# Kernel optimization log

Measured on AMD Instinct MI355X. Metric: run time of the kernel, lower is better.

## Reference

```python
import jax, jax.numpy as jnp
import numpy as np

B, S, D = 1, 2048, 1024
F = 1408            # expert intermediate dim
E = 16              # num experts
K = 2               # top_k
CAP_FACTOR = 1.25


def _mlp(h, wg, wu, wd):
    # DeepSeek-style gated MLP (SwiGLU, no bias)
    return (jax.nn.silu(h @ wg) * (h @ wu)) @ wd


def setup_inputs() -> dict:
    key = jax.random.key(0)
    ks = jax.random.split(key, 10)
    sd = 0.02
    return {
        "x": jax.random.normal(ks[0], (B, S, D), jnp.float32),
        "router_w": jax.random.normal(ks[1], (D, E), jnp.float32) * sd,
        "router_b": jnp.zeros((E,), jnp.float32),
        "w_gate": jax.random.normal(ks[2], (E, D, F), jnp.float32) * sd,
        "w_up": jax.random.normal(ks[3], (E, D, F), jnp.float32) * sd,
        "w_down": jax.random.normal(ks[4], (E, F, D), jnp.float32) * sd,
        "sw_gate": jax.random.normal(ks[5], (D, F), jnp.float32) * sd,
        "sw_up": jax.random.normal(ks[6], (D, F), jnp.float32) * sd,
        "sw_down": jax.random.normal(ks[7], (F, D), jnp.float32) * sd,
    }


def reference(x, router_w, router_b, w_gate, w_up, w_down, sw_gate, sw_up, sw_down):
    b, s, d = x.shape
    N = b * s
    NK = N * K
    C = int(np.ceil(CAP_FACTOR * NK / E))  # per-expert capacity

    x_tokens = x.reshape(N, d)

    # Router: softmax -> top-k -> renormalize
    logits = x_tokens @ router_w + router_b           # [N, E]
    probs = jax.nn.softmax(logits, axis=-1)
    vals, idx = jax.lax.top_k(probs, K)               # [N, K]
    vals = vals / (jnp.sum(vals, axis=-1, keepdims=True) + 1e-9)
    idx_flat = idx.reshape(NK)                        # int expert ids
    vals_flat = vals.reshape(NK)

    # Position within each expert's buffer = rank in flattened (token, k) order.
    # Same math as (cumsum(one_hot)*one_hot).sum(-1)-1 in the original.
    oh_e = jax.nn.one_hot(idx_flat, E, dtype=x.dtype)             # [NK, E] (small)
    pos = (jnp.cumsum(oh_e, axis=0) * oh_e).sum(axis=1) - 1       # [NK]
    within = (pos < C).astype(x.dtype)                            # capacity mask
    pos_c = jnp.clip(pos, 0, C - 1).astype(jnp.int32)

    # Dispatch: scatter tokens into per-expert buffers. Positions are unique
    # per expert, so scatter-add equals the dense one-hot einsum exactly.
    token_ids = jnp.arange(NK) // K
    x_pair = x_tokens[token_ids] * within[:, None]                # [NK, D]
    expert_inputs = jnp.zeros((E, C, d), x.dtype).at[idx_flat, pos_c].add(x_pair)

    # Grouped expert MLPs
    expert_outputs = jax.vmap(_mlp)(expert_inputs, w_gate, w_up, w_down)  # [E, C, D]

    # Combine: gather back and weight by renormalized router probs
    gathered = expert_outputs[idx_flat, pos_c] * (vals_flat * within)[:, None]
    output_tokens = gathered.reshape(N, K, d).sum(axis=1)         # [N, D]

    return x + _mlp(x, sw_gate, sw_up, sw_down) + output_tokens.reshape(b, s, d)
```

## Files before the change

### kernel.cpp

```cpp
#include <hip/hip_runtime.h>
#include <hip/hip_bf16.h>

#define TOKENS 2048
#define DIM    1024
#define FDIM   1408
#define NEXP   16
#define NK     (TOKENS * 2)
#define CAP    320
#define RPAD   384

typedef __attribute__((ext_vector_type(4))) float f32x4;
typedef __attribute__((ext_vector_type(8))) short s16x8;
typedef __attribute__((ext_vector_type(4))) short s16x4;

__device__ __forceinline__ short f2bf(float f) {
    unsigned int u = __float_as_uint(f);
    u += 0x7FFFu + ((u >> 16) & 1u);
    return (short)(u >> 16);
}
__device__ __forceinline__ float bf2f(short s) {
    return __uint_as_float(((unsigned int)(unsigned short)s) << 16);
}

#define GLDS16(gp, lp) __builtin_amdgcn_global_load_lds(                     \
    (const __attribute__((address_space(1))) unsigned int*)(gp),             \
    (__attribute__((address_space(3))) unsigned int*)(lp), 16, 0, 0)

struct GSeg {
    const short* A; long aStride; int aRpad;
    const short* B0; const short* B1; long bStride;
    short* Out; long oStride; int oRpad;
    const int* cnt; int Mb, Nb, N, K, nblocks;
};
struct WSeg { const float* in; short* out; int K, N, mats, nblocks; };

__device__ void wchunk_dev(const WSeg& W, int bid)
{
    const int spm = W.K >> 3;
    const int mat = bid / spm, s = bid % spm;
    const float* in  = W.in  + (size_t)mat * W.K * W.N + (size_t)s * 8 * W.N;
    short* out = W.out + (size_t)mat * W.K * W.N + (size_t)s * W.N * 8;
    const int t = threadIdx.x;
    const int iters = (W.N + 511) >> 9;
    for (int it = 0; it < iters; it++) {
        const int n = it * 512 + 2 * t;
        if (n >= W.N) break;
        const float* src = in + n;
        s16x8 o0, o1;
#pragma unroll
        for (int j = 0; j < 8; j++) {
            float2 v = *(const float2*)(src + (size_t)j * W.N);
            o0[j] = f2bf(v.x);
            o1[j] = f2bf(v.y);
        }
        *(s16x8*)(out + (size_t)n * 8)     = o0;
        *(s16x8*)(out + (size_t)n * 8 + 8) = o1;
    }
}

__global__ __launch_bounds__(256) void router_kernel(
    const float* __restrict__ x, const float* __restrict__ rw,
    const float* __restrict__ rb, int* __restrict__ idx_flat,
    float* __restrict__ vals_flat)
{
    __shared__ float lg[16][17];
    const int t  = threadIdx.x;
    const int tl = t >> 4;
    const int e  = t & 15;
    const int token = blockIdx.x * 16 + tl;
    const float* xr = x + (size_t)token * DIM;

    float acc = 0.f;
    for (int d4 = 0; d4 < DIM / 4; d4++) {
        float4 xv = *(const float4*)(xr + d4 * 4);
        acc += xv.x * rw[(d4 * 4 + 0) * NEXP + e];
        acc += xv.y * rw[(d4 * 4 + 1) * NEXP + e];
        acc += xv.z * rw[(d4 * 4 + 2) * NEXP + e];
        acc += xv.w * rw[(d4 * 4 + 3) * NEXP + e];
    }
    lg[tl][e] = acc + rb[e];
    __syncthreads();

    if (t < 16) {
        float l[16];
#pragma unroll
        for (int j = 0; j < 16; j++) l[j] = lg[t][j];
        float m = l[0];
#pragma unroll
        for (int j = 1; j < 16; j++) m = fmaxf(m, l[j]);
        float p[16], den = 0.f;
#pragma unroll
        for (int j = 0; j < 16; j++) { p[j] = __expf(l[j] - m); den += p[j]; }
        int i1 = -1; float b1 = -1e30f;
#pragma unroll
        for (int j = 0; j < 16; j++) if (p[j] > b1) { b1 = p[j]; i1 = j; }
        int i2 = -1; float b2 = -1e30f;
#pragma unroll
        for (int j = 0; j < 16; j++) if (j != i1 && p[j] > b2) { b2 = p[j]; i2 = j; }
        float v1 = b1 / den, v2 = b2 / den;
        float s = v1 + v2 + 1e-9f;
        int tok = blockIdx.x * 16 + t;
        idx_flat[tok * 2 + 0] = i1;
        idx_flat[tok * 2 + 1] = i2;
        vals_flat[tok * 2 + 0] = v1 / s;
        vals_flat[tok * 2 + 1] = v2 / s;
    }
}

__global__ void scan_kernel(const int* __restrict__ idx_flat,
                            const float* __restrict__ vals,
                            int* __restrict__ dst, float* __restrict__ wgt,
                            int* __restrict__ cnt)
{
    const int lane = threadIdx.x;
    int base[16];
#pragma unroll
    for (int e = 0; e < 16; e++) base[e] = 0;

    for (int c = 0; c < NK / 64; c++) {
        int i = c * 64 + lane;
        int e = idx_flat[i];
        unsigned long long m[16];
#pragma unroll
        for (int ee = 0; ee < 16; ee++) m[ee] = __ballot(e == ee);
        unsigned long long mym = 0ULL; int myb = 0;
#pragma unroll
        for (int ee = 0; ee < 16; ee++) {
            bool sel = (e == ee);
            mym = sel ? m[ee] : mym;
            myb = sel ? base[ee] : myb;
        }
        int pos = myb + (int)__popcll(mym & ((1ULL << lane) - 1ULL));
        bool within = pos < CAP;
        dst[i] = within ? (e * RPAD + pos) : -1;
        wgt[i] = within ? vals[i] : 0.f;
#pragma unroll
        for (int ee = 0; ee < 16; ee++) base[ee] += (int)__popcll(m[ee]);
    }
    if (lane < 16) cnt[lane] = base[lane] < CAP ? base[lane] : CAP;
}

__device__ void xconv_dev(const float* __restrict__ x, short* __restrict__ xb, int bid)
{
    const int token = bid * 2 + (threadIdx.x >> 7);
    const int c = threadIdx.x & 127;
    const float* src = x + (size_t)token * DIM + c * 8;
    float4 v0 = *(const float4*)(src);
    float4 v1 = *(const float4*)(src + 4);
    s16x8 o;
    o[0] = f2bf(v0.x); o[1] = f2bf(v0.y); o[2] = f2bf(v0.z); o[3] = f2bf(v0.w);
    o[4] = f2bf(v1.x); o[5] = f2bf(v1.y); o[6] = f2bf(v1.z); o[7] = f2bf(v1.w);
    *(s16x8*)(xb + (size_t)c * (TOKENS * 8) + (size_t)token * 8) = o;
}

__device__ void scatter_dev(const float* __restrict__ x, const int* __restrict__ dst,
                            const int* __restrict__ idx_flat, short* __restrict__ ex,
                            int bid)
{
    const int i = bid * 2 + (threadIdx.x >> 7);
    const int d0 = dst[i];
    if (d0 < 0) return;
    const int e = idx_flat[i];
    const int pos = d0 - e * RPAD;
    const int token = i >> 1;
    const int c = threadIdx.x & 127;
    const float* src = x + (size_t)token * DIM + c * 8;
    float4 v0 = *(const float4*)(src);
    float4 v1 = *(const float4*)(src + 4);
    s16x8 o;
    o[0] = f2bf(v0.x); o[1] = f2bf(v0.y); o[2] = f2bf(v0.z); o[3] = f2bf(v0.w);
    o[4] = f2bf(v1.x); o[5] = f2bf(v1.y); o[6] = f2bf(v1.z); o[7] = f2bf(v1.w);
    *(s16x8*)(ex + (size_t)e * (DIM * RPAD) + (size_t)c * (RPAD * 8) +
              (size_t)pos * 8) = o;
}

__global__ __launch_bounds__(256) void mid_kernel(
    WSeg w0, WSeg w1, WSeg w2, WSeg w3,
    const float* __restrict__ x, short* __restrict__ xb,
    const int* __restrict__ dst, const int* __restrict__ idx_flat,
    short* __restrict__ ex)
{
    int bid = blockIdx.x;
    if (bid < w0.nblocks) { wchunk_dev(w0, bid); return; }
    bid -= w0.nblocks;
    if (bid < w1.nblocks) { wchunk_dev(w1, bid); return; }
    bid -= w1.nblocks;
    if (bid < w2.nblocks) { wchunk_dev(w2, bid); return; }
    bid -= w2.nblocks;
    if (bid < w3.nblocks) { wchunk_dev(w3, bid); return; }
    bid -= w3.nblocks;
    if (bid < TOKENS / 2) { xconv_dev(x, xb, bid); return; }
    bid -= TOKENS / 2;
    scatter_dev(x, dst, idx_flat, ex, bid);
}

template <int NMAT>
__device__ void gemm_dev(const GSeg& S, int bid)
{
    constexpr int BUFS = 4096 * (1 + NMAT);
    __shared__ short lds[2 * BUFS];

    const int cpx = S.nblocks >> 3;
    const int lid = (bid & 7) * cpx + (bid >> 3);
    const int mb  = lid % S.Mb;
    const int t1  = lid / S.Mb;
    const int nb  = t1 % S.Nb;
    const int g   = t1 / S.Nb;
    const int m0 = mb * 128, n0 = nb * 128;
    if (S.cnt != nullptr && m0 >= S.cnt[g]) return;

    const int tid = threadIdx.x, lane = tid & 63, w = tid >> 6;
    const int wr = w >> 1, wc = w & 1, ln = lane & 15, kg = lane >> 4;

    const int N = S.N, K = S.K;
    const short* Ag  = S.A  + (size_t)g * S.aStride + (size_t)m0 * 8;
    const short* Bg0 = S.B0 + (size_t)g * S.bStride + (size_t)n0 * 8;
    const short* Bg1 = nullptr;
    if constexpr (NMAT == 2) Bg1 = S.B1 + (size_t)g * S.bStride + (size_t)n0 * 8;

    const size_t aR8 = (size_t)S.aRpad * 8;
    const size_t n8  = (size_t)N * 8;

    const int srow = tid & 127, sslab = tid >> 7;
    const short* aS0 = Ag  + sslab * aR8 + srow * 8;
    const short* aS1 = Ag  + (2 + sslab) * aR8 + srow * 8;
    const short* bS00 = Bg0 + sslab * n8 + srow * 8;
    const short* bS01 = Bg0 + (2 + sslab) * n8 + srow * 8;
    const short* bS10 = nullptr, *bS11 = nullptr;
    if constexpr (NMAT == 2) {
        bS10 = Bg1 + sslab * n8 + srow * 8;
        bS11 = Bg1 + (2 + sslab) * n8 + srow * 8;
    }

    const int dA0 = w * 512, dA1 = 2048 + w * 512;

    auto STG = [&](int buf, int ks) {
        const size_t ka = (size_t)ks * 4 * aR8;
        const size_t kb = (size_t)ks * 4 * n8;
        short* base = lds + buf * BUFS;
        GLDS16(aS0 + ka,  base + dA0);
        GLDS16(aS1 + ka,  base + dA1);
        GLDS16(bS00 + kb, base + 4096 + dA0);
        GLDS16(bS01 + kb, base + 4096 + dA1);
        if constexpr (NMAT == 2) {
            GLDS16(bS10 + kb, base + 8192 + dA0);
            GLDS16(bS11 + kb, base + 8192 + dA1);
        }
    };

    const int aO = kg * 1024 + (wr * 64 + ln) * 8;
    const int bO = kg * 1024 + (wc * 64 + ln) * 8;

    f32x4 acc[NMAT][4][4] = {};

    const int nt = K / 32;
    STG(0, 0); STG(1, 1);
    int cur = 0;
    for (int ks = 0; ks < nt; ks++) {
        if (ks + 1 < nt) {
            if constexpr (NMAT == 2) asm volatile("s_waitcnt vmcnt(6)" ::: "memory");
            else                     asm volatile("s_waitcnt vmcnt(4)" ::: "memory");
        } else {
            asm volatile("s_waitcnt vmcnt(0)" ::: "memory");
        }
        __builtin_amdgcn_s_barrier();
        __builtin_amdgcn_sched_barrier(0);

        const short* base = lds + cur * BUFS;
        s16x8 af[4];
#pragma unroll
        for (int m = 0; m < 4; m++)
            af[m] = *(const s16x8*)(base + aO + m * 128);
        s16x8 bf[NMAT][4];
#pragma unroll
        for (int mat = 0; mat < NMAT; mat++)
#pragma unroll
            for (int nf = 0; nf < 4; nf++)
                bf[mat][nf] = *(const s16x8*)(base + 4096 + mat * 4096 + bO + nf * 128);

        __builtin_amdgcn_s_setprio(1);
#pragma unroll
        for (int nf = 0; nf < 4; nf++)
#pragma unroll
            for (int m = 0; m < 4; m++)
#pragma unroll
                for (int mat = 0; mat < NMAT; mat++)
                    acc[mat][m][nf] = __builtin_amdgcn_mfma_f32_16x16x32_bf16(
                        af[m], bf[mat][nf], acc[mat][m][nf], 0, 0, 0);
        __builtin_amdgcn_s_setprio(0);
        __builtin_amdgcn_sched_barrier(0);
        __builtin_amdgcn_s_barrier();

        if (ks + 2 < nt) STG(cur, ks + 2);
        cur ^= 1;
    }

#pragma unroll
    for (int m = 0; m < 4; m++) {
#pragma unroll
        for (int nf = 0; nf < 4; nf++) {
            const int row = m0 + wr * 64 + m * 16 + kg * 4;
            const int col = n0 + wc * 64 + nf * 16 + ln;
#pragma unroll
            for (int j = 0; j < 4; j++) {
                if constexpr (NMAT == 2) {
                    float gv = acc[0][m][nf][j];
                    float uv = acc[1][m][nf][j];
                    float v = gv / (1.f + __expf(-gv)) * uv;
                    S.Out[(size_t)g * S.oStride + (size_t)(col >> 3) * (S.oRpad * 8) +
                          (size_t)(row + j) * 8 + (col & 7)] = f2bf(v);
                } else {
                    S.Out[(size_t)g * S.oStride + (size_t)(row + j) * N + col] =
                        f2bf(acc[0][m][nf][j]);
                }
            }
        }
    }
}

__global__ __launch_bounds__(256, 2) void gateup_kernel(GSeg s0, GSeg s1,
                                                        WSeg w0, WSeg w1)
{
    int bid = blockIdx.x;
    if (bid < s0.nblocks) { gemm_dev<2>(s0, bid); return; }
    bid -= s0.nblocks;
    if (bid < s1.nblocks) { gemm_dev<2>(s1, bid); return; }
    bid -= s1.nblocks;
    if (bid < w0.nblocks) { wchunk_dev(w0, bid); return; }
    bid -= w0.nblocks;
    wchunk_dev(w1, bid);
}

__global__ __launch_bounds__(256, 2) void down_kernel(GSeg s0, GSeg s1)
{
    int bid = blockIdx.x;
    if (bid < s0.nblocks) { gemm_dev<1>(s0, bid); return; }
    bid -= s0.nblocks;
    gemm_dev<1>(s1, bid);
}

__global__ __launch_bounds__(256) void combine_kernel(
    const float* __restrict__ x, const short* __restrict__ shout,
    const short* __restrict__ eout, const int* __restrict__ dst,
    const float* __restrict__ wgt, float* __restrict__ out)
{
    const int t = blockIdx.x;
    const int d = threadIdx.x * 4;
    size_t o = (size_t)t * DIM + d;
    float4 xv = *(const float4*)(x + o);
    s16x4 sv = *(const s16x4*)(shout + o);
    float r0 = xv.x + bf2f(sv[0]);
    float r1 = xv.y + bf2f(sv[1]);
    float r2 = xv.z + bf2f(sv[2]);
    float r3 = xv.w + bf2f(sv[3]);
#pragma unroll
    for (int k = 0; k < 2; k++) {
        int di = dst[t * 2 + k];
        if (di >= 0) {
            float wv = wgt[t * 2 + k];
            s16x4 ev = *(const s16x4*)(eout + (size_t)di * DIM + d);
            r0 += wv * bf2f(ev[0]);
            r1 += wv * bf2f(ev[1]);
            r2 += wv * bf2f(ev[2]);
            r3 += wv * bf2f(ev[3]);
        }
    }
    float4 rv = {r0, r1, r2, r3};
    *(float4*)(out + o) = rv;
}

extern "C" void kernel_launch(void* const* d_in, const int* in_sizes, int n_in,
                              void* d_out, int out_size, void* d_ws, size_t ws_size,
                              hipStream_t stream)
{
    const float* x   = (const float*)d_in[0];
    const float* rw  = (const float*)d_in[1];
    const float* rb  = (const float*)d_in[2];
    const float* wg  = (const float*)d_in[3];
    const float* wu  = (const float*)d_in[4];
    const float* wd  = (const float*)d_in[5];
    const float* swg = (const float*)d_in[6];
    const float* swu = (const float*)d_in[7];
    const float* swd = (const float*)d_in[8];
    float* out = (float*)d_out;

    char* wp = (char*)d_ws;
    auto alloc = [&](size_t b) { char* p = wp; wp += (b + 255) & ~(size_t)255; return p; };
    int*   idx_flat = (int*)alloc((size_t)NK * 4);
    float* vals     = (float*)alloc((size_t)NK * 4);
    int*   dst      = (int*)alloc((size_t)NK * 4);
    float* wgt      = (float*)alloc((size_t)NK * 4);
    int*   cnt      = (int*)alloc(64);
    short* xb       = (short*)alloc((size_t)TOKENS * DIM * 2);
    short* ex       = (short*)alloc((size_t)NEXP * RPAD * DIM * 2);
    short* acte     = (short*)alloc((size_t)NEXP * RPAD * FDIM * 2);
    short* acts     = (short*)alloc((size_t)TOKENS * FDIM * 2);
    short* eout     = (short*)alloc((size_t)NEXP * RPAD * DIM * 2);
    short* shout    = (short*)alloc((size_t)TOKENS * DIM * 2);
    short* wgC      = (short*)alloc((size_t)NEXP * DIM * FDIM * 2);
    short* wuC      = (short*)alloc((size_t)NEXP * DIM * FDIM * 2);
    short* wdC      = (short*)alloc((size_t)NEXP * DIM * FDIM * 2);
    short* swgC     = (short*)alloc((size_t)DIM * FDIM * 2);
    short* swuC     = (short*)alloc((size_t)DIM * FDIM * 2);
    short* swdC     = (short*)alloc((size_t)DIM * FDIM * 2);

    WSeg Wg  = {wg,  wgC,  DIM,  FDIM, NEXP, NEXP * (DIM / 8)};
    WSeg Wu  = {wu,  wuC,  DIM,  FDIM, NEXP, NEXP * (DIM / 8)};
    WSeg Wsg = {swg, swgC, DIM,  FDIM, 1,    DIM / 8};
    WSeg Wsu = {swu, swuC, DIM,  FDIM, 1,    DIM / 8};
    WSeg Wd  = {wd,  wdC,  FDIM, DIM,  NEXP, NEXP * (FDIM / 8)};
    WSeg Wsd = {swd, swdC, FDIM, DIM,  1,    FDIM / 8};

    router_kernel<<<TOKENS / 16, 256, 0, stream>>>(x, rw, rb, idx_flat, vals);
    scan_kernel<<<1, 64, 0, stream>>>(idx_flat, vals, dst, wgt, cnt);

    const int mid_blocks = Wg.nblocks + Wu.nblocks + Wsg.nblocks + Wsu.nblocks
                         + TOKENS / 2 + NK / 2;
    mid_kernel<<<mid_blocks, 256, 0, stream>>>(Wg, Wu, Wsg, Wsu,
                                               x, xb, dst, idx_flat, ex);

    GSeg segGE = {ex, (long)RPAD * DIM, RPAD, wgC, wuC, (long)DIM * FDIM,
                  acte, (long)RPAD * FDIM, RPAD, cnt, 3, 11, FDIM, DIM, 3 * 11 * NEXP};
    GSeg segGS = {xb, 0L, TOKENS, swgC, swuC, 0L,
                  acts, 0L, TOKENS, nullptr, 16, 11, FDIM, DIM, 16 * 11};
    gateup_kernel<<<segGE.nblocks + segGS.nblocks + Wd.nblocks + Wsd.nblocks,
                    256, 0, stream>>>(segGE, segGS, Wd, Wsd);

    GSeg segDE = {acte, (long)RPAD * FDIM, RPAD, wdC, nullptr, (long)DIM * FDIM,
                  eout, (long)RPAD * DIM, 0, cnt, 3, 8, DIM, FDIM, 3 * 8 * NEXP};
    GSeg segDS = {acts, 0L, TOKENS, swdC, nullptr, 0L,
                  shout, 0L, 0, nullptr, 16, 8, DIM, FDIM, 16 * 8};
    down_kernel<<<segDE.nblocks + segDS.nblocks, 256, 0, stream>>>(segDE, segDS);

    combine_kernel<<<TOKENS, 256, 0, stream>>>(x, shout, eout, dst, wgt, out);
}
```

Baseline: 249.5 us.

## Triple-buffer gate/up GEMM, add 64-row down GEMM tile, vectorize weight conversion

The gate/up GEMM moves from double to triple LDS buffering, with deeper prefetch and adjusted vmcnt waits. The down projection gets a new 64x128-tile GEMM with launch bounds allowing 4 blocks per CU, which doubles the block count to improve occupancy and load balance over the expert-capacity rows. Weight fp32-to-bf16 conversion now uses float4 loads and packed bf16 conversion. Trade-offs are more LDS per gate/up block, which may reduce occupancy, and less reuse per tile in the down GEMM.

New measurement: 254.3 us. About the same (+1.9%).

```diff
diff --git a/kernel.cpp b/kernel.cpp
--- a/kernel.cpp
+++ b/kernel.cpp
@@ -21,17 +21,28 @@
 __device__ __forceinline__ float bf2f(short s) {
     return __uint_as_float(((unsigned int)(unsigned short)s) << 16);
 }
+__device__ __forceinline__ unsigned int f2bf_pk(float lo, float hi) {
+    union { __hip_bfloat162 h; unsigned int u; } c;
+    c.h = __float22bfloat162_rn(make_float2(lo, hi));
+    return c.u;
+}
 
 #define GLDS16(gp, lp) __builtin_amdgcn_global_load_lds(                     \
     (const __attribute__((address_space(1))) unsigned int*)(gp),             \
     (__attribute__((address_space(3))) unsigned int*)(lp), 16, 0, 0)
 
-struct GSeg {
+struct GSegW {
     const short* A; long aStride; int aRpad;
     const short* B0; const short* B1; long bStride;
     short* Out; long oStride; int oRpad;
     const int* cnt; int Mb, Nb, N, K, nblocks;
 };
+struct GSegB {
+    const short* A; long aStride; int aRpad;
+    const short* B0; long bStride;
+    short* Out; long oStride;
+    const int* cnt; int Mb, Nb, N, K, nblocks;
+};
 struct WSeg { const float* in; short* out; int K, N, mats, nblocks; };
 
 __device__ void wchunk_dev(const WSeg& W, int bid)
@@ -41,20 +52,20 @@
     const float* in  = W.in  + (size_t)mat * W.K * W.N + (size_t)s * 8 * W.N;
     short* out = W.out + (size_t)mat * W.K * W.N + (size_t)s * W.N * 8;
     const int t = threadIdx.x;
-    const int iters = (W.N + 511) >> 9;
-    for (int it = 0; it < iters; it++) {
-        const int n = it * 512 + 2 * t;
-        if (n >= W.N) break;
-        const float* src = in + n;
-        s16x8 o0, o1;
-#pragma unroll
-        for (int j = 0; j < 8; j++) {
-            float2 v = *(const float2*)(src + (size_t)j * W.N);
-            o0[j] = f2bf(v.x);
-            o1[j] = f2bf(v.y);
-        }
-        *(s16x8*)(out + (size_t)n * 8)     = o0;
-        *(s16x8*)(out + (size_t)n * 8 + 8) = o1;
+    for (int n0 = 4 * t; n0 < W.N; n0 += 1024) {
+        f32x4 v[8];
+#pragma unroll
+        for (int j = 0; j < 8; j++)
+            v[j] = *(const f32x4*)(in + (size_t)j * W.N + n0);
+#pragma unroll
+        for (int c = 0; c < 4; c++) {
+            uint4 o;
+            o.x = f2bf_pk(v[0][c], v[1][c]);
+            o.y = f2bf_pk(v[2][c], v[3][c]);
+            o.z = f2bf_pk(v[4][c], v[5][c]);
+            o.w = f2bf_pk(v[6][c], v[7][c]);
+            *(uint4*)(out + (size_t)(n0 + c) * 8) = o;
+        }
     }
 }
 
@@ -174,7 +185,7 @@
               (size_t)pos * 8) = o;
 }
 
-__global__ __launch_bounds__(256) void mid_kernel(
+__global__ __launch_bounds__(256) void prep_kernel(
     WSeg w0, WSeg w1, WSeg w2, WSeg w3,
     const float* __restrict__ x, short* __restrict__ xb,
     const int* __restrict__ dst, const int* __restrict__ idx_flat,
@@ -195,10 +206,10 @@
 }
 
 template <int NMAT>
-__device__ void gemm_dev(const GSeg& S, int bid)
+__device__ void gemm_glds128_dev(const GSegW& S, int bid)
 {
     constexpr int BUFS = 4096 * (1 + NMAT);
-    __shared__ short lds[2 * BUFS];
+    __shared__ short lds[3 * BUFS];
 
     const int cpx = S.nblocks >> 3;
     const int lid = (bid & 7) * cpx + (bid >> 3);
@@ -211,8 +222,8 @@
 
     const int tid = threadIdx.x, lane = tid & 63, w = tid >> 6;
     const int wr = w >> 1, wc = w & 1, ln = lane & 15, kg = lane >> 4;
-
     const int N = S.N, K = S.K;
+
     const short* Ag  = S.A  + (size_t)g * S.aStride + (size_t)m0 * 8;
     const short* Bg0 = S.B0 + (size_t)g * S.bStride + (size_t)n0 * 8;
     const short* Bg1 = nullptr;
@@ -222,11 +233,11 @@
     const size_t n8  = (size_t)N * 8;
 
     const int srow = tid & 127, sslab = tid >> 7;
-    const short* aS0 = Ag  + sslab * aR8 + srow * 8;
-    const short* aS1 = Ag  + (2 + sslab) * aR8 + srow * 8;
+    const short* aS0 = Ag + sslab * aR8 + srow * 8;
+    const short* aS1 = Ag + (2 + sslab) * aR8 + srow * 8;
     const short* bS00 = Bg0 + sslab * n8 + srow * 8;
     const short* bS01 = Bg0 + (2 + sslab) * n8 + srow * 8;
-    const short* bS10 = nullptr, *bS11 = nullptr;
+    const short *bS10 = nullptr, *bS11 = nullptr;
     if constexpr (NMAT == 2) {
         bS10 = Bg1 + sslab * n8 + srow * 8;
         bS11 = Bg1 + (2 + sslab) * n8 + srow * 8;
@@ -252,12 +263,15 @@
     const int bO = kg * 1024 + (wc * 64 + ln) * 8;
 
     f32x4 acc[NMAT][4][4] = {};
-
     const int nt = K / 32;
-    STG(0, 0); STG(1, 1);
-    int cur = 0;
+    STG(0, 0); STG(1, 1); STG(2, 2);
+    int bb = 0;
     for (int ks = 0; ks < nt; ks++) {
-        if (ks + 1 < nt) {
+        const int rem = nt - 1 - ks;
+        if (rem >= 2) {
+            if constexpr (NMAT == 2) asm volatile("s_waitcnt vmcnt(12)" ::: "memory");
+            else                     asm volatile("s_waitcnt vmcnt(8)"  ::: "memory");
+        } else if (rem == 1) {
             if constexpr (NMAT == 2) asm volatile("s_waitcnt vmcnt(6)" ::: "memory");
             else                     asm volatile("s_waitcnt vmcnt(4)" ::: "memory");
         } else {
@@ -266,7 +280,7 @@
         __builtin_amdgcn_s_barrier();
         __builtin_amdgcn_sched_barrier(0);
 
-        const short* base = lds + cur * BUFS;
+        const short* base = lds + bb * BUFS;
         s16x8 af[4];
 #pragma unroll
         for (int m = 0; m < 4; m++)
@@ -291,8 +305,8 @@
         __builtin_amdgcn_sched_barrier(0);
         __builtin_amdgcn_s_barrier();
 
-        if (ks + 2 < nt) STG(cur, ks + 2);
-        cur ^= 1;
+        if (ks + 3 < nt) STG(bb, ks + 3);
+        bb = (bb == 2) ? 0 : bb + 1;
     }
 
 #pragma unroll
@@ -318,25 +332,113 @@
     }
 }
 
-__global__ __launch_bounds__(256, 2) void gateup_kernel(GSeg s0, GSeg s1,
+__device__ void gemm_glds64_dev(const GSegB& S, int bid)
+{
+    constexpr int BUFS = 6144;
+    __shared__ short lds[2 * BUFS];
+
+    const int cpx = S.nblocks >> 3;
+    const int lid = (bid & 7) * cpx + (bid >> 3);
+    const int mb  = lid % S.Mb;
+    const int t1  = lid / S.Mb;
+    const int nb  = t1 % S.Nb;
+    const int g   = t1 / S.Nb;
+    const int m0 = mb * 64, n0 = nb * 128;
+    if (S.cnt != nullptr && m0 >= S.cnt[g]) return;
+
+    const int tid = threadIdx.x, lane = tid & 63, w = tid >> 6;
+    const int wr = w >> 1, wc = w & 1, ln = lane & 15, kg = lane >> 4;
+    const int N = S.N, K = S.K;
+
+    const short* Ag = S.A  + (size_t)g * S.aStride + (size_t)m0 * 8;
+    const short* Bg = S.B0 + (size_t)g * S.bStride + (size_t)n0 * 8;
+
+    const size_t aR8 = (size_t)S.aRpad * 8;
+    const size_t n8  = (size_t)N * 8;
+
+    const short* aS  = Ag + (size_t)(tid >> 6) * aR8 + (size_t)(tid & 63) * 8;
+    const short* bS0 = Bg + (size_t)(tid >> 7) * n8 + (size_t)(tid & 127) * 8;
+    const short* bS1 = Bg + (size_t)((tid >> 7) + 2) * n8 + (size_t)(tid & 127) * 8;
+
+    const int dA  = w * 512;
+    const int dB0 = 2048 + w * 512;
+    const int dB1 = 4096 + w * 512;
+
+    auto STG = [&](int buf, int ks) {
+        const size_t ka = (size_t)ks * 4 * aR8;
+        const size_t kb = (size_t)ks * 4 * n8;
+        short* base = lds + buf * BUFS;
+        GLDS16(aS + ka,  base + dA);
+        GLDS16(bS0 + kb, base + dB0);
+        GLDS16(bS1 + kb, base + dB1);
+    };
+
+    const int aO = kg * 512 + (wr * 32 + ln) * 8;
+    const int bO = 2048 + kg * 1024 + (wc * 64 + ln) * 8;
+
+    f32x4 acc[2][4] = {};
+    const int nt = K / 32;
+    STG(0, 0); STG(1, 1);
+    int cur = 0;
+    for (int ks = 0; ks < nt; ks++) {
+        if (ks + 1 < nt) asm volatile("s_waitcnt vmcnt(3)" ::: "memory");
+        else             asm volatile("s_waitcnt vmcnt(0)" ::: "memory");
+        __builtin_amdgcn_s_barrier();
+        __builtin_amdgcn_sched_barrier(0);
+
+        const short* base = lds + cur * BUFS;
+        s16x8 af[2];
+        af[0] = *(const s16x8*)(base + aO);
+        af[1] = *(const s16x8*)(base + aO + 128);
+        s16x8 bf[4];
+#pragma unroll
+        for (int nf = 0; nf < 4; nf++)
+            bf[nf] = *(const s16x8*)(base + bO + nf * 128);
+
+#pragma unroll
+        for (int nf = 0; nf < 4; nf++)
+#pragma unroll
+            for (int m = 0; m < 2; m++)
+                acc[m][nf] = __builtin_amdgcn_mfma_f32_16x16x32_bf16(
+                    af[m], bf[nf], acc[m][nf], 0, 0, 0);
+
+        __builtin_amdgcn_sched_barrier(0);
+        __builtin_amdgcn_s_barrier();
+        if (ks + 2 < nt) STG(cur, ks + 2);
+        cur ^= 1;
+    }
+
+#pragma unroll
+    for (int m = 0; m < 2; m++) {
+#pragma unroll
+        for (int nf = 0; nf < 4; nf++) {
+            const int row = m0 + wr * 32 + m * 16 + kg * 4;
+            const int col = n0 + wc * 64 + nf * 16 + ln;
+#pragma unroll
+            for (int j = 0; j < 4; j++)
+                S.Out[(size_t)g * S.oStride + (size_t)(row + j) * N + col] =
+                    f2bf(acc[m][nf][j]);
+        }
+    }
+}
+
+__global__ __launch_bounds__(256, 2) void gateup_kernel(GSegW s0, GSegW s1,
                                                         WSeg w0, WSeg w1)
 {
     int bid = blockIdx.x;
-    if (bid < s0.nblocks) { gemm_dev<2>(s0, bid); return; }
+    if (bid < s0.nblocks) { gemm_glds128_dev<2>(s0, bid); return; }
     bid -= s0.nblocks;
-    if (bid < s1.nblocks) { gemm_dev<2>(s1, bid); return; }
+    if (bid < s1.nblocks) { gemm_glds128_dev<2>(s1, bid); return; }
     bid -= s1.nblocks;
     if (bid < w0.nblocks) { wchunk_dev(w0, bid); return; }
-    bid -= w0.nblocks;
-    wchunk_dev(w1, bid);
-}
-
-__global__ __launch_bounds__(256, 2) void down_kernel(GSeg s0, GSeg s1)
+    wchunk_dev(w1, bid - w0.nblocks);
+}
+
+__global__ __launch_bounds__(256, 4) void down_kernel(GSegB s0, GSegB s1)
 {
     int bid = blockIdx.x;
-    if (bid < s0.nblocks) { gemm_dev<1>(s0, bid); return; }
-    bid -= s0.nblocks;
-    gemm_dev<1>(s1, bid);
+    if (bid < s0.nblocks) { gemm_glds64_dev(s0, bid); return; }
+    gemm_glds64_dev(s1, bid - s0.nblocks);
 }
 
 __global__ __launch_bounds__(256) void combine_kernel(
@@ -404,32 +506,31 @@
     short* swuC     = (short*)alloc((size_t)DIM * FDIM * 2);
     short* swdC     = (short*)alloc((size_t)DIM * FDIM * 2);
 
-    WSeg Wg  = {wg,  wgC,  DIM,  FDIM, NEXP, NEXP * (DIM / 8)};
-    WSeg Wu  = {wu,  wuC,  DIM,  FDIM, NEXP, NEXP * (DIM / 8)};
-    WSeg Wsg = {swg, swgC, DIM,  FDIM, 1,    DIM / 8};
-    WSeg Wsu = {swu, swuC, DIM,  FDIM, 1,    DIM / 8};
-    WSeg Wd  = {wd,  wdC,  FDIM, DIM,  NEXP, NEXP * (FDIM / 8)};
-    WSeg Wsd = {swd, swdC, FDIM, DIM,  1,    FDIM / 8};
-
     router_kernel<<<TOKENS / 16, 256, 0, stream>>>(x, rw, rb, idx_flat, vals);
     scan_kernel<<<1, 64, 0, stream>>>(idx_flat, vals, dst, wgt, cnt);
 
-    const int mid_blocks = Wg.nblocks + Wu.nblocks + Wsg.nblocks + Wsu.nblocks
-                         + TOKENS / 2 + NK / 2;
-    mid_kernel<<<mid_blocks, 256, 0, stream>>>(Wg, Wu, Wsg, Wsu,
-                                               x, xb, dst, idx_flat, ex);
-
-    GSeg segGE = {ex, (long)RPAD * DIM, RPAD, wgC, wuC, (long)DIM * FDIM,
-                  acte, (long)RPAD * FDIM, RPAD, cnt, 3, 11, FDIM, DIM, 3 * 11 * NEXP};
-    GSeg segGS = {xb, 0L, TOKENS, swgC, swuC, 0L,
-                  acts, 0L, TOKENS, nullptr, 16, 11, FDIM, DIM, 16 * 11};
+    WSeg Wg  = {wg,  wgC,  DIM, FDIM, NEXP, NEXP * (DIM / 8)};
+    WSeg Wu  = {wu,  wuC,  DIM, FDIM, NEXP, NEXP * (DIM / 8)};
+    WSeg Wsg = {swg, swgC, DIM, FDIM, 1,    DIM / 8};
+    WSeg Wsu = {swu, swuC, DIM, FDIM, 1,    DIM / 8};
+    const int prep_blocks = Wg.nblocks + Wu.nblocks + Wsg.nblocks + Wsu.nblocks
+                          + TOKENS / 2 + NK / 2;
+    prep_kernel<<<prep_blocks, 256, 0, stream>>>(Wg, Wu, Wsg, Wsu,
+                                                 x, xb, dst, idx_flat, ex);
+
+    GSegW segGE = {ex, (long)RPAD * DIM, RPAD, wgC, wuC, (long)DIM * FDIM,
+                   acte, (long)RPAD * FDIM, RPAD, cnt, 3, 11, FDIM, DIM, 3 * 11 * NEXP};
+    GSegW segGS = {xb, 0L, TOKENS, swgC, swuC, 0L,
+                   acts, 0L, TOKENS, nullptr, 16, 11, FDIM, DIM, 16 * 11};
+    WSeg Wd  = {wd,  wdC,  FDIM, DIM, NEXP, NEXP * (FDIM / 8)};
+    WSeg Wsd = {swd, swdC, FDIM, DIM, 1,    FDIM / 8};
     gateup_kernel<<<segGE.nblocks + segGS.nblocks + Wd.nblocks + Wsd.nblocks,
                     256, 0, stream>>>(segGE, segGS, Wd, Wsd);
 
-    GSeg segDE = {acte, (long)RPAD * FDIM, RPAD, wdC, nullptr, (long)DIM * FDIM,
-                  eout, (long)RPAD * DIM, 0, cnt, 3, 8, DIM, FDIM, 3 * 8 * NEXP};
-    GSeg segDS = {acts, 0L, TOKENS, swdC, nullptr, 0L,
-                  shout, 0L, 0, nullptr, 16, 8, DIM, FDIM, 16 * 8};
+    GSegB segDE = {acte, (long)RPAD * FDIM, RPAD, wdC, (long)DIM * FDIM,
+                   eout, (long)RPAD * DIM, cnt, 6, 8, DIM, FDIM, 6 * 8 * NEXP};
+    GSegB segDS = {acts, 0L, TOKENS, swdC, 0L,
+                   shout, 0L, nullptr, 32, 8, DIM, FDIM, 32 * 8};
     down_kernel<<<segDE.nblocks + segDS.nblocks, 256, 0, stream>>>(segDE, segDS);
 
     combine_kernel<<<TOKENS, 256, 0, stream>>>(x, shout, eout, dst, wgt, out);
```
